# Kernel optimization log

Hardware: AMD Instinct MI355X
Metric: run time of the kernel (lower is better)

Reference implementation:

```python
import jax, jax.numpy as jnp
import numpy as np

KH, KW, STRIDE = 3, 3, 1

def setup_inputs() -> dict:
    key = jax.random.key(0)
    x = jax.random.normal(key, (32, 64, 64, 64), dtype=jnp.float32)  # [B, C, H, W]
    return {"x": x}

def unfold(x, Kh, Kw, stride):
    B, C, H, W = x.shape
    Ho = H - (Kh - 1)  # number of row positions (loop bound in original)
    Wo = W - (Kw - 1)
    # Gather all patches with a small fixed Kh*Kw loop (vectorized over B,C,Ho,Wo).
    # Original flattens each patch [C, Kh, Kw] -> C*Kh*Kw (channel-major),
    # and enumerates positions row-major (i outer, j inner).
    slabs = [x[:, :, i * stride:i * stride + Ho, j * stride:j * stride + Wo]
             for i in range(Kh) for j in range(Kw)]          # each [B, C, Ho, Wo]
    p = jnp.stack(slabs, axis=2)                              # [B, C, Kh*Kw, Ho, Wo]
    return p.reshape(B, C * Kh * Kw, Ho * Wo)                 # [B, C*Kh*Kw, L]

def reference(x):
    return unfold(x, KH, KW, STRIDE)
```

## Files before the change

kernel.cpp:

```cpp
#include <hip/hip_runtime.h>


#define B 32
#define C 64
#define H 64
#define W 64
#define HO 62
#define WO 62
#define L (HO * WO)
#define L4 (L / 4)
#define KK 9

__device__ __forceinline__ int sw(int p) { return p + (p >> 5); }

__global__ __launch_bounds__(256) void unfold_kernel(
    const float* __restrict__ x, float* __restrict__ out) {
    __shared__ float tile[H * W + (H * W) / 32];

    const int c   = blockIdx.x;
    const int b   = blockIdx.y;
    const int tid = threadIdx.x;

    const float4* __restrict__ src =
        (const float4*)(x + (((size_t)(b * C + c)) << 12));
#pragma unroll
    for (int r = 0; r < 4; ++r) {
        const int p4 = tid + r * 256;
        float4 v = src[p4];
        const int p = p4 * 4;
        tile[sw(p)]     = v.x;
        tile[sw(p + 1)] = v.y;
        tile[sw(p + 2)] = v.z;
        tile[sw(p + 3)] = v.w;
    }
    __syncthreads();

    float4* __restrict__ dst =
        (float4*)out + (size_t)(b * C + c) * KK * L4;

#pragma unroll
    for (int k = 0; k < KK; ++k) {
        const int i = k / 3;
        const int j = k - i * 3;
        const int base = i * W + j;
        for (int t = tid; t < L4; t += 256) {
            const int l0 = t * 4;
            int ho = l0 / WO;
            int wo = l0 - ho * WO;
            int addr = base + ho * W + wo;
            float r[4];
#pragma unroll
            for (int q = 0; q < 4; ++q) {
                r[q] = tile[sw(addr)];
                ++addr;
                ++wo;
                if (wo == WO) { wo = 0; addr += (W - WO); }
            }
            float4 v;
            v.x = r[0]; v.y = r[1]; v.z = r[2]; v.w = r[3];
            dst[k * L4 + t] = v;
        }
    }
}

extern "C" void kernel_launch(void* const* d_in, const int* in_sizes, int n_in,
                              void* d_out, int out_size, void* d_ws, size_t ws_size,
                              hipStream_t stream) {
    const float* x = (const float*)d_in[0];
    float* out = (float*)d_out;

    dim3 block(256, 1, 1);
    dim3 grid(C, B, 1);
    unfold_kernel<<<grid, block, 0, stream>>>(x, out);
}
```

Measured before the change: 313.8 us.

## Restructure unfold to float2 stores with all nine taps per position

Removes the padded shared-memory swizzle and loads the tile with direct float4 LDS writes. Each thread now computes a position pair once and writes all nine kernel taps as float2 stores, avoiding the per-element wraparound logic. It also raises the occupancy hint. The cost is narrower global stores, which may lower write efficiency on a store-bound kernel.

```diff
diff --git a/kernel.cpp b/kernel.cpp
--- a/kernel.cpp
+++ b/kernel.cpp
@@ -8,14 +8,12 @@
 #define HO 62
 #define WO 62
 #define L (HO * WO)
-#define L4 (L / 4)
+#define L2 (L / 2)
 #define KK 9
 
-__device__ __forceinline__ int sw(int p) { return p + (p >> 5); }
-
-__global__ __launch_bounds__(256) void unfold_kernel(
+__global__ __launch_bounds__(256, 8) void unfold_kernel(
     const float* __restrict__ x, float* __restrict__ out) {
-    __shared__ float tile[H * W + (H * W) / 32];
+    __shared__ float tile[H * W];
 
     const int c   = blockIdx.x;
     const int b   = blockIdx.y;
@@ -23,42 +21,31 @@
 
     const float4* __restrict__ src =
         (const float4*)(x + (((size_t)(b * C + c)) << 12));
+    float4* __restrict__ t4 = (float4*)tile;
 #pragma unroll
     for (int r = 0; r < 4; ++r) {
-        const int p4 = tid + r * 256;
-        float4 v = src[p4];
-        const int p = p4 * 4;
-        tile[sw(p)]     = v.x;
-        tile[sw(p + 1)] = v.y;
-        tile[sw(p + 2)] = v.z;
-        tile[sw(p + 3)] = v.w;
+        t4[tid + r * 256] = src[tid + r * 256];
     }
     __syncthreads();
 
-    float4* __restrict__ dst =
-        (float4*)out + (size_t)(b * C + c) * KK * L4;
+    float2* __restrict__ dst2 =
+        (float2*)out + (size_t)(b * C + c) * KK * L2;
+
+    for (int pe = tid; pe < L2; pe += 256) {
+        const int l  = pe * 2;
+        const int ho = l / WO;
+        const int wo = l - ho * WO;
+        const int a  = ho * W + wo;
 
 #pragma unroll
-    for (int k = 0; k < KK; ++k) {
-        const int i = k / 3;
-        const int j = k - i * 3;
-        const int base = i * W + j;
-        for (int t = tid; t < L4; t += 256) {
-            const int l0 = t * 4;
-            int ho = l0 / WO;
-            int wo = l0 - ho * WO;
-            int addr = base + ho * W + wo;
-            float r[4];
+        for (int i = 0; i < 3; ++i) {
 #pragma unroll
-            for (int q = 0; q < 4; ++q) {
-                r[q] = tile[sw(addr)];
-                ++addr;
-                ++wo;
-                if (wo == WO) { wo = 0; addr += (W - WO); }
+            for (int j = 0; j < 3; ++j) {
+                float2 v;
+                v.x = tile[a + i * W + j];
+                v.y = tile[a + i * W + j + 1];
+                dst2[(i * 3 + j) * L2 + pe] = v;
             }
-            float4 v;
-            v.x = r[0]; v.y = r[1]; v.z = r[2]; v.w = r[3];
-            dst[k * L4 + t] = v;
         }
     }
 }
```

Result: no change. 314.8 us (+0.3%).
